# Kernel tuning notes

Measured on AMD Instinct MI355X. Metric: run time of the kernel, lower is better.

The kernel has to match this reference:

```python
import jax, jax.numpy as jnp
import numpy as np

DM = 768            # d_model
DI = 1536           # d_inner = expand * d_model
P = 64              # headdim
H = DI // P         # 24 heads
N = 64              # d_state (Mamba2Simple default)
K = 4               # d_conv
CONVD = DI + 2 * N  # 1664
D_IN_PROJ = 2 * DI + 2 * N + H  # 3224
BATCH = 2
NVAL = 1024
L = NVAL
EPS = 1e-5

# static tail_order / swap_order index (transpose the rows x cols token grid, reversed)
_rows = int(NVAL ** 0.5)
_t = np.arange(NVAL).reshape(_rows, -1).T
_t = NVAL - 1 - _t
TAIL = _t.reshape(-1)
SEQ = jnp.asarray(np.concatenate([np.arange(L - NVAL), TAIL + (L - NVAL)]))


def _make_params(key, prefix):
    ks = jax.random.split(key, 6)
    dt = jnp.exp(jax.random.uniform(ks[2], (H,), minval=np.log(1e-3), maxval=np.log(1e-1)))
    return {
        prefix + 'ln_w': jnp.ones(DM, jnp.float32),
        prefix + 'ln_b': jnp.zeros(DM, jnp.float32),
        prefix + 'in_w': jax.random.normal(ks[0], (D_IN_PROJ, DM), jnp.float32) * 0.02,
        prefix + 'conv_w': jax.random.normal(ks[1], (CONVD, K), jnp.float32) * 0.1,
        prefix + 'conv_b': jnp.zeros(CONVD, jnp.float32),
        prefix + 'dt_bias': jnp.log(jnp.expm1(dt)),  # inverse softplus of dt in [1e-3, 1e-1]
        prefix + 'A_log': jnp.log(jax.random.uniform(ks[3], (H,), minval=1.0, maxval=16.0)),
        prefix + 'D': jnp.ones(H, jnp.float32),
        prefix + 'norm_w': jnp.ones(DI, jnp.float32),
        prefix + 'out_w': jax.random.normal(ks[4], (DM, DI), jnp.float32) * 0.02,
    }


def setup_inputs() -> dict:
    key = jax.random.key(0)
    k1, k2, k3 = jax.random.split(key, 3)
    inp = {'x': jax.random.normal(k1, (BATCH, L, DM), dtype=jnp.float32)}
    inp.update(_make_params(k2, 'f_'))
    inp.update(_make_params(k3, 'b_'))
    return inp


def _layernorm(x, w, b):
    m = jnp.mean(x, -1, keepdims=True)
    v = jnp.mean((x - m) ** 2, -1, keepdims=True)
    return (x - m) * jax.lax.rsqrt(v + EPS) * w + b


def _mamba2(x, in_w, conv_w, conv_b, dt_bias, A_log, Dp, norm_w, out_w):
    Bsz, Lseq, _ = x.shape
    zxbcdt = x @ in_w.T                                   # [B,L,3224]
    z, xBC, dt = jnp.split(zxbcdt, [DI, DI + CONVD], axis=-1)
    dt = jax.nn.softplus(dt + dt_bias)                    # [B,L,H]
    # causal depthwise conv1d over channels
    xc = jnp.transpose(xBC, (0, 2, 1))                    # [B,C,L]
    xc = jax.lax.conv_general_dilated(xc, conv_w[:, None, :], (1,), [(K - 1, 0)],
                                      feature_group_count=CONVD)
    xBC = jax.nn.silu(jnp.transpose(xc, (0, 2, 1)) + conv_b)
    xs, Bm, Cm = jnp.split(xBC, [DI, DI + N], axis=-1)
    xs = xs.reshape(Bsz, Lseq, H, P)
    A = -jnp.exp(A_log)                                   # [H], negative

    def step(S, inp):
        dt_t, x_t, B_t, C_t = inp                         # [B,H],[B,H,P],[B,N],[B,N]
        dA = jnp.exp(dt_t * A)                            # [B,H]
        S = S * dA[..., None, None] + dt_t[..., None, None] * B_t[:, None, :, None] * x_t[:, :, None, :]
        y = jnp.einsum('bn,bhnp->bhp', C_t, S)
        return S, y

    S0 = jnp.zeros((Bsz, H, N, P), x.dtype)
    ins = (jnp.moveaxis(dt, 1, 0), jnp.moveaxis(xs, 1, 0),
           jnp.moveaxis(Bm, 1, 0), jnp.moveaxis(Cm, 1, 0))
    _, ys = jax.lax.scan(step, S0, ins)
    y = jnp.moveaxis(ys, 0, 1) + Dp[None, None, :, None] * xs  # D skip, [B,L,H,P]
    y = y.reshape(Bsz, Lseq, DI)
    # RMSNormGated: gate then rmsnorm
    y = y * jax.nn.silu(z)
    y = y * jax.lax.rsqrt(jnp.mean(y * y, -1, keepdims=True) + EPS) * norm_w
    return y @ out_w.T


def _wrap(x, ln_w, ln_b, *mp):
    return x + _mamba2(_layernorm(x, ln_w, ln_b), *mp)


def reference(x,
              f_ln_w, f_ln_b, f_in_w, f_conv_w, f_conv_b, f_dt_bias, f_A_log, f_D, f_norm_w, f_out_w,
              b_ln_w, b_ln_b, b_in_w, b_conv_w, b_conv_b, b_dt_bias, b_A_log, b_D, b_norm_w, b_out_w):
    left_right = _wrap(x, f_ln_w, f_ln_b, f_in_w, f_conv_w, f_conv_b, f_dt_bias, f_A_log, f_D, f_norm_w, f_out_w)
    xs = x[:, SEQ]
    down_up = _wrap(xs, b_ln_w, b_ln_b, b_in_w, b_conv_w, b_conv_b, b_dt_bias, b_A_log, b_D, b_norm_w, b_out_w)
    down_up = down_up[:, SEQ]
    return left_right + down_up
```

## Files before the change

kernel.cpp:

```cpp
#include <hip/hip_runtime.h>
#include <cstdint>

#define DM    768
#define DI    1536
#define PP    64
#define HH    24
#define NN    64
#define CONVD 1664
#define DINP  3224
#define NP1   3328
#define LL    1024
#define ROWS  2048
#define EPSF  1e-5f
#define NCHUNK 16
#define CLEN   64

typedef unsigned short ushortT;
typedef __attribute__((ext_vector_type(8))) __bf16 bf16x8;
typedef __attribute__((ext_vector_type(8))) unsigned short ushort8;
typedef __attribute__((ext_vector_type(4))) float f32x4;

__device__ __forceinline__ int seqmap(int t) { return 1023 - 32 * (t & 31) - (t >> 5); }

__device__ __forceinline__ ushortT f2bf(float f) {
  union { float f; unsigned u; } v; v.f = f;
  unsigned r = v.u + 0x7FFF + ((v.u >> 16) & 1);
  return (ushortT)(r >> 16);
}
__device__ __forceinline__ float bf2f(ushortT b) {
  union { unsigned u; float f; } v; v.u = ((unsigned)b) << 16;
  return v.f;
}

__device__ __forceinline__ void gload_lds16(const void* g, void* l) {
  __builtin_amdgcn_global_load_lds((const __attribute__((address_space(1))) void*)g,
                                   (__attribute__((address_space(3))) void*)l, 16, 0, 0);
}

#define SWZ(r, c) ((r) * 64 + ((c) ^ (((r) & 7) << 3)))
#define SWZ64(r, c) ((r) * 64 + ((c) ^ (((r) & 7) << 3)))

__global__ __launch_bounds__(256) void cvt_all_kernel(
    const float* __restrict__ fw1, const float* __restrict__ bw1,
    const float* __restrict__ fw2, const float* __restrict__ bw2,
    ushortT* __restrict__ WP1, ushortT* __restrict__ W2) {
  const long NW1 = (long)NP1 * DM, SW1 = (long)DINP * DM, NW2 = (long)DM * DI;
  const long tot8 = (2 * NW1 + 2 * NW2) >> 3;
  for (long i8 = (long)blockIdx.x * 256 + threadIdx.x; i8 < tot8; i8 += (long)gridDim.x * 256) {
    long i = i8 << 3;
    const float* src = nullptr;
    ushortT* dst;
    if (i < NW1) {
      if (i < SW1) src = fw1 + i;
      dst = WP1 + i;
    } else if (i < 2 * NW1) {
      long j = i - NW1;
      if (j < SW1) src = bw1 + j;
      dst = WP1 + i;
    } else if (i < 2 * NW1 + NW2) {
      long j = i - 2 * NW1;
      src = fw2 + j;
      dst = W2 + j;
    } else {
      long j = i - 2 * NW1 - NW2;
      src = bw2 + j;
      dst = W2 + NW2 + j;
    }
    ushort8 o = {};
    if (src) {
      float4 a = *(const float4*)src;
      float4 b2 = *(const float4*)(src + 4);
      o[0] = f2bf(a.x);  o[1] = f2bf(a.y);  o[2] = f2bf(a.z);  o[3] = f2bf(a.w);
      o[4] = f2bf(b2.x); o[5] = f2bf(b2.y); o[6] = f2bf(b2.z); o[7] = f2bf(b2.w);
    }
    *(ushort8*)dst = o;
  }
}

__global__ __launch_bounds__(256) void ln_kernel(const float* __restrict__ x,
    const float* __restrict__ wf, const float* __restrict__ bf_,
    const float* __restrict__ wb, const float* __restrict__ bb,
    ushortT* __restrict__ xln) {
  __shared__ float lds[4];
  int bid = blockIdx.x;
  int dir = bid >> 11, row = bid & 2047;
  int b = row >> 10, t = row & 1023;
  int st = dir ? seqmap(t) : t;
  const float* xr = x + (size_t)(b * 1024 + st) * DM;
  const float* w = dir ? wb : wf;
  const float* bia = dir ? bb : bf_;
  int tid = threadIdx.x;
  float v0 = xr[tid], v1 = xr[tid + 256], v2 = xr[tid + 512];
  float s = v0 + v1 + v2;
  #pragma unroll
  for (int o = 32; o; o >>= 1) s += __shfl_xor(s, o, 64);
  if ((tid & 63) == 0) lds[tid >> 6] = s;
  __syncthreads();
  float mean = (lds[0] + lds[1] + lds[2] + lds[3]) * (1.f / 768.f);
  __syncthreads();
  float d0 = v0 - mean, d1 = v1 - mean, d2 = v2 - mean;
  float q = d0 * d0 + d1 * d1 + d2 * d2;
  #pragma unroll
  for (int o = 32; o; o >>= 1) q += __shfl_xor(q, o, 64);
  if ((tid & 63) == 0) lds[tid >> 6] = q;
  __syncthreads();
  float var = (lds[0] + lds[1] + lds[2] + lds[3]) * (1.f / 768.f);
  float rs = rsqrtf(var + EPSF);
  ushortT* orow = xln + (size_t)bid * DM;
  orow[tid]       = f2bf(d0 * rs * w[tid]       + bia[tid]);
  orow[tid + 256] = f2bf(d1 * rs * w[tid + 256] + bia[tid + 256]);
  orow[tid + 512] = f2bf(d2 * rs * w[tid + 512] + bia[tid + 512]);
}

template<int MODE>
__global__ __launch_bounds__(256) void gemm_bf16(
    const ushortT* __restrict__ Aall, const ushortT* __restrict__ Ball,
    float* __restrict__ Cfall, ushortT* __restrict__ Cball,
    int K, int lda, int ldb, int ldc, long sA, long sB, long sCf, long sCb) {
  __shared__ ushortT sA2[2][128 * 64];
  __shared__ ushortT sB2[2][128 * 64];
  int gx = gridDim.x, gy = gridDim.y;
  int nwg = gx * gy * gridDim.z;
  int lid = blockIdx.x + gx * (blockIdx.y + gy * blockIdx.z);
  int cpx = nwg >> 3;
  int swz = (lid & 7) * cpx + (lid >> 3);
  int bx = swz % gx;
  int rest = swz / gx;
  int by = rest % gy, bz = rest / gy;
  const ushortT* A = Aall + (size_t)bz * sA;
  const ushortT* B = Ball + (size_t)bz * sB;
  int tid = threadIdx.x, lane = tid & 63, w = tid >> 6;
  int wm = w >> 1, wn = w & 1;
  int m0 = by * 128, n0 = bx * 128;
  int rA8 = lane >> 3;
  int cSw = ((lane & 7) << 3) ^ (((lane >> 3) & 7) << 3);
  f32x4 acc[4][4] = {};
  const int NT = K >> 6;
  int fr = lane & 15, kq = lane >> 4;

  auto STAGE = [&](int bf, int kt) {
    int kc = kt * 64 + cSw;
    #pragma unroll
    for (int c2 = 0; c2 < 4; ++c2) {
      int q = w * 4 + c2;
      gload_lds16(A + (size_t)(m0 + q * 8 + rA8) * lda + kc, &sA2[bf][q * 512]);
    }
    #pragma unroll
    for (int c2 = 0; c2 < 4; ++c2) {
      int q = w * 4 + c2;
      gload_lds16(B + (size_t)(n0 + q * 8 + rA8) * ldb + kc, &sB2[bf][q * 512]);
    }
  };

  STAGE(0, 0);
  int cur = 0;
  for (int kt = 0; kt < NT; ++kt) {
    if (kt + 1 < NT) {
      STAGE(cur ^ 1, kt + 1);
      asm volatile("s_waitcnt vmcnt(8)" ::: "memory");
    } else {
      asm volatile("s_waitcnt vmcnt(0)" ::: "memory");
    }
    __builtin_amdgcn_s_barrier();
    __builtin_amdgcn_sched_barrier(0);
    #pragma unroll
    for (int ks = 0; ks < 2; ++ks) {
      int kb = ks * 32 + kq * 8;
      bf16x8 af[4], bfr[4];
      #pragma unroll
      for (int i = 0; i < 4; ++i)
        af[i] = *(const bf16x8*)&sA2[cur][SWZ64(wm * 64 + i * 16 + fr, kb)];
      #pragma unroll
      for (int j = 0; j < 4; ++j)
        bfr[j] = *(const bf16x8*)&sB2[cur][SWZ64(wn * 64 + j * 16 + fr, kb)];
      #pragma unroll
      for (int i = 0; i < 4; ++i)
        #pragma unroll
        for (int j = 0; j < 4; ++j)
          acc[i][j] = __builtin_amdgcn_mfma_f32_16x16x32_bf16(af[i], bfr[j], acc[i][j], 0, 0, 0);
    }
    asm volatile("s_waitcnt lgkmcnt(0)" ::: "memory");
    __builtin_amdgcn_sched_barrier(0);
    __builtin_amdgcn_s_barrier();
    cur ^= 1;
  }
  int cr = (lane >> 4) * 4, cc = lane & 15;
  if (MODE == 1 && n0 >= 3200) {
    float* Cf = Cfall + (size_t)bz * sCf;
    #pragma unroll
    for (int i = 0; i < 4; ++i)
      #pragma unroll
      for (int j = 0; j < 4; ++j) {
        float* Cp = Cf + (size_t)(m0 + wm * 64 + i * 16 + cr) * 128 + (wn * 64 + j * 16 + cc);
        #pragma unroll
        for (int r = 0; r < 4; ++r) Cp[(size_t)r * 128] = acc[i][j][r];
      }
  } else {
    ushortT* Cb = Cball + (size_t)bz * sCb;
    #pragma unroll
    for (int i = 0; i < 4; ++i)
      #pragma unroll
      for (int j = 0; j < 4; ++j) {
        ushortT* Cp = Cb + (size_t)(m0 + wm * 64 + i * 16 + cr) * ldc + (n0 + wn * 64 + j * 16 + cc);
        #pragma unroll
        for (int r = 0; r < 4; ++r) Cp[(size_t)r * ldc] = f2bf(acc[i][j][r]);
      }
  }
}

__global__ __launch_bounds__(256) void conv_dt_kernel(const ushortT* __restrict__ zxb,
    const float* __restrict__ dtt,
    const float* __restrict__ cwf, const float* __restrict__ cbf,
    const float* __restrict__ cwb, const float* __restrict__ cbb,
    const float* __restrict__ dtbf, const float* __restrict__ alogf,
    const float* __restrict__ dtbb, const float* __restrict__ alogb,
    ushortT* __restrict__ xcb, float* __restrict__ dts, float* __restrict__ lda_) {
  int bid = blockIdx.x;
  int dir = bid >> 11, row = bid & 2047;
  int t = row & 1023;
  const float* cw   = dir ? cwb : cwf;
  const float* cb   = dir ? cbb : cbf;
  const float* dtb  = dir ? dtbb : dtbf;
  const float* alog = dir ? alogb : alogf;
  const ushortT* zrow = zxb + (size_t)bid * NP1;
  int tid = threadIdx.x;
  if (tid < HH) {
    float raw = dtt[(size_t)bid * 128 + tid] + dtb[tid];
    float dtv = raw > 20.f ? raw : log1pf(expf(raw));
    dts[(size_t)bid * HH + tid] = dtv;
    lda_[(size_t)bid * HH + tid] = -expf(alog[tid]) * dtv;
  }
  ushortT* xrow = xcb + (size_t)bid * CONVD;
  for (int c = tid; c < CONVD; c += 256) {
    float acc = cb[c];
    #pragma unroll
    for (int k = 0; k < 4; ++k) {
      int tt = t - 3 + k;
      if (tt >= 0) acc += bf2f(zrow[(long)(k - 3) * NP1 + 1536 + c]) * cw[c * 4 + k];
    }
    xrow[c] = f2bf(acc / (1.f + expf(-acc)));
  }
}

__global__ __launch_bounds__(256) void ssd_chunk_kernel(const ushortT* __restrict__ xcb,
    const float* __restrict__ dts, const float* __restrict__ lda_,
    ushortT* __restrict__ yb, ushortT* __restrict__ slocb, float* __restrict__ cwg,
    ushortT* __restrict__ cbg) {
  __shared__ ushortT sCb[4096];
  __shared__ ushortT sBb[4096];
  __shared__ ushortT sBT[4096];
  __shared__ ushortT sXT[4096];
  __shared__ ushortT sMb[4096];
  __shared__ float clog[64];
  __shared__ float dt64[64];
  __shared__ float wv64[64];
  int gh = blockIdx.x;
  int c  = blockIdx.y;
  int dir = gh / 48;
  int rem = gh % 48;
  int b = rem / 24, h = rem % 24;
  int tid = threadIdx.x, lane = tid & 63;
  int w = tid >> 6;
  size_t rowbase = ((size_t)dir * 2 + b) * 1024;
  size_t trow = rowbase + (size_t)c * CLEN;

  #pragma unroll
  for (int it2 = 0; it2 < 2; ++it2) {
    int idx2 = it2 * 256 + tid;
    int r = idx2 >> 3, c8 = (idx2 & 7) << 3;
    const ushortT* xrow = xcb + (trow + r) * CONVD;
    *(ushort8*)&sCb[SWZ(r, c8)] = *(const ushort8*)&xrow[1600 + c8];
    *(ushort8*)&sBb[SWZ(r, c8)] = *(const ushort8*)&xrow[1536 + c8];
  }
  #pragma unroll
  for (int it = 0; it < 16; ++it) {
    int idx = it * 256 + tid;
    int r = idx >> 6, cc = idx & 63;
    sXT[SWZ(cc, r)] = xcb[(trow + r) * CONVD + h * 64 + cc];
  }
  if (tid < 64) {
    float ld = lda_[(trow + tid) * HH + h];
    float dtv = dts[(trow + tid) * HH + h];
    float v = ld;
    #pragma unroll
    for (int o = 1; o < 64; o <<= 1) {
      float u = __shfl_up(v, o, 64);
      if (tid >= o) v += u;
    }
    float tot = __shfl(v, 63, 64);
    clog[tid] = v;
    dt64[tid] = dtv;
    wv64[tid] = dtv * __expf(tot - v);
    cwg[(trow + tid) * HH + h] = __expf(v);
  }
  __syncthreads();

  if (h == 0) {
    ushortT* dst = cbg + ((size_t)((dir * 2 + b) * NCHUNK + c)) * 4096;
    for (int idx = tid; idx < 4096; idx += 256) dst[idx] = sCb[idx];
  }

  int fr = lane & 15, kq = lane >> 4;

  #pragma unroll
  for (int it = 0; it < 16; ++it) {
    int idx = it * 256 + tid;
    int s = idx >> 6, n = idx & 63;
    float bv = bf2f(sBb[SWZ(s, n)]) * wv64[s];
    sBT[SWZ(n, s)] = f2bf(bv);
  }
  f32x4 accG[4] = {};
  #pragma unroll
  for (int kt = 0; kt < 2; ++kt) {
    int kk = kt * 32 + kq * 8;
    bf16x8 af = *(const bf16x8*)&sCb[SWZ(w * 16 + fr, kk)];
    #pragma unroll
    for (int j = 0; j < 4; ++j) {
      bf16x8 bf_ = *(const bf16x8*)&sBb[SWZ(j * 16 + fr, kk)];
      accG[j] = __builtin_amdgcn_mfma_f32_16x16x32_bf16(af, bf_, accG[j], 0, 0, 0);
    }
  }
  #pragma unroll
  for (int j = 0; j < 4; ++j) {
    int s = j * 16 + fr;
    float cls = clog[s], dtv = dt64[s];
    #pragma unroll
    for (int r = 0; r < 4; ++r) {
      int t = w * 16 + kq * 4 + r;
      float dec = (s <= t) ? __expf(clog[t] - cls) * dtv : 0.f;
      sMb[SWZ(t, s)] = f2bf(accG[j][r] * dec);
    }
  }
  __syncthreads();

  f32x4 accY[4] = {}, accS[4] = {};
  #pragma unroll
  for (int kt = 0; kt < 2; ++kt) {
    int kk = kt * 32 + kq * 8;
    bf16x8 aM = *(const bf16x8*)&sMb[SWZ(w * 16 + fr, kk)];
    bf16x8 aB = *(const bf16x8*)&sBT[SWZ(w * 16 + fr, kk)];
    #pragma unroll
    for (int j = 0; j < 4; ++j) {
      bf16x8 bx = *(const bf16x8*)&sXT[SWZ(j * 16 + fr, kk)];
      accY[j] = __builtin_amdgcn_mfma_f32_16x16x32_bf16(aM, bx, accY[j], 0, 0, 0);
      accS[j] = __builtin_amdgcn_mfma_f32_16x16x32_bf16(aB, bx, accS[j], 0, 0, 0);
    }
  }
  ushortT* spb = slocb + ((size_t)gh * NCHUNK + c) * 4096;
  #pragma unroll
  for (int j = 0; j < 4; ++j) {
    #pragma unroll
    for (int r = 0; r < 4; ++r) {
      int t = w * 16 + kq * 4 + r;
      int p = j * 16 + fr;
      yb[(trow + t) * DI + h * 64 + p] = f2bf(accY[j][r]);
      spb[t * 64 + p] = f2bf(accS[j][r]);
    }
  }
}

__global__ __launch_bounds__(256) void chunk_prefix_kernel(
    const ushortT* __restrict__ slocb, const float* __restrict__ cwg,
    ushortT* __restrict__ sinitb) {
  __shared__ float ldsT[64 * 65];
  int gh = blockIdx.x;
  int dir = gh / 48;
  int rem = gh % 48;
  int b = rem / 24, h = rem % 24;
  int tid = threadIdx.x;
  size_t rowbase = ((size_t)dir * 2 + b) * 1024;
  float R[16];
  #pragma unroll
  for (int j = 0; j < 16; ++j) R[j] = 0.f;
  for (int c = 1; c < NCHUNK; ++c) {
    float W = cwg[(rowbase + (size_t)c * CLEN - 1) * HH + h];
    const ushortT* slot = slocb + ((size_t)gh * NCHUNK + (c - 1)) * 4096;
    #pragma unroll
    for (int j = 0; j < 16; ++j) {
      int idx = j * 256 + tid, n = idx >> 6, p = idx & 63;
      R[j] = __builtin_fmaf(R[j], W, bf2f(slot[idx]));
      ldsT[n * 65 + p] = R[j];
    }
    __syncthreads();
    ushortT* outp = sinitb + ((size_t)gh * (NCHUNK - 1) + (c - 1)) * 4096;
    #pragma unroll
    for (int j = 0; j < 16; ++j) {
      int idx = j * 256 + tid, p = idx >> 6, n = idx & 63;
      outp[SWZ(p, n)] = f2bf(ldsT[n * 65 + p]);
    }
    __syncthreads();
  }
}

__global__ __launch_bounds__(256) void fixup_kernel(
    const ushortT* __restrict__ cbg, const ushortT* __restrict__ sinitb,
    const float* __restrict__ cwg, ushortT* __restrict__ yib) {
  __shared__ ushortT sCb[4096];
  __shared__ ushortT sST[4096];
  int gh = blockIdx.x;
  int c = blockIdx.y + 1;
  int dir = gh / 48;
  int rem = gh % 48;
  int b = rem / 24, h = rem % 24;
  int tid = threadIdx.x, lane = tid & 63, w = tid >> 6;
  size_t rowbase = ((size_t)dir * 2 + b) * 1024;
  size_t trow = rowbase + (size_t)c * CLEN;
  const ushortT* cbSrc = cbg + ((size_t)((dir * 2 + b) * NCHUNK + c)) * 4096;
  const ushortT* stSrc = sinitb + ((size_t)gh * (NCHUNK - 1) + (c - 1)) * 4096;
  #pragma unroll
  for (int ph = 0; ph < 2; ++ph) {
    int base = ph * 2048 + w * 512;
    gload_lds16(cbSrc + base + lane * 8, &sCb[base]);
    gload_lds16(stSrc + base + lane * 8, &sST[base]);
  }
  __syncthreads();
  int fr = lane & 15, kq = lane >> 4;
  f32x4 accY[4] = {};
  #pragma unroll
  for (int kt = 0; kt < 2; ++kt) {
    int kk = kt * 32 + kq * 8;
    bf16x8 aC = *(const bf16x8*)&sCb[SWZ(w * 16 + fr, kk)];
    #pragma unroll
    for (int j = 0; j < 4; ++j) {
      bf16x8 bS = *(const bf16x8*)&sST[SWZ(j * 16 + fr, kk)];
      accY[j] = __builtin_amdgcn_mfma_f32_16x16x32_bf16(aC, bS, accY[j], 0, 0, 0);
    }
  }
  float cwv[4];
  #pragma unroll
  for (int r = 0; r < 4; ++r)
    cwv[r] = cwg[(trow + w * 16 + kq * 4 + r) * HH + h];
  #pragma unroll
  for (int j = 0; j < 4; ++j)
    #pragma unroll
    for (int r = 0; r < 4; ++r) {
      int t = w * 16 + kq * 4 + r, p = j * 16 + fr;
      yib[(trow + t) * DI + h * 64 + p] = f2bf(accY[j][r] * cwv[r]);
    }
}

__global__ __launch_bounds__(256) void gate_norm_kernel(
    const ushortT* __restrict__ yb, const ushortT* __restrict__ yib,
    const ushortT* __restrict__ zxb, const ushortT* __restrict__ xcb,
    const float* __restrict__ Df, const float* __restrict__ Db,
    const float* __restrict__ nwf, const float* __restrict__ nwb,
    ushortT* __restrict__ yn) {
  __shared__ float lds[4];
  int bid = blockIdx.x;
  int dir = bid >> 11;
  int t = bid & 1023;
  const float* Dp = dir ? Db : Df;
  const float* nw = dir ? nwb : nwf;
  int tid = threadIdx.x;
  bool act = tid < 192;
  int c0 = tid * 8;
  float v[8];
  float ss = 0.f;
  if (act) {
    ushort8 yv8 = *(const ushort8*)&yb[(size_t)bid * DI + c0];
    ushort8 zv8 = *(const ushort8*)&zxb[(size_t)bid * NP1 + c0];
    ushort8 xv8 = *(const ushort8*)&xcb[(size_t)bid * CONVD + c0];
    ushort8 yi8 = {};
    bool hasI = (t >= CLEN);
    if (hasI) yi8 = *(const ushort8*)&yib[(size_t)bid * DI + c0];
    float Dv = Dp[c0 >> 6];
    #pragma unroll
    for (int e = 0; e < 8; ++e) {
      float yv = bf2f(yv8[e]) + (hasI ? bf2f(yi8[e]) : 0.f) + Dv * bf2f(xv8[e]);
      float zv = bf2f(zv8[e]);
      yv *= zv / (1.f + expf(-zv));
      v[e] = yv;
      ss += yv * yv;
    }
  }
  #pragma unroll
  for (int o = 32; o; o >>= 1) ss += __shfl_xor(ss, o, 64);
  if ((tid & 63) == 0) lds[tid >> 6] = ss;
  __syncthreads();
  float ms = (lds[0] + lds[1] + lds[2] + lds[3]) * (1.f / 1536.f);
  float sc = rsqrtf(ms + EPSF);
  if (act) {
    ushort8 o8;
    #pragma unroll
    for (int e = 0; e < 8; ++e) o8[e] = f2bf(v[e] * sc * nw[c0 + e]);
    *(ushort8*)&yn[(size_t)bid * DI + c0] = o8;
  }
}

__global__ __launch_bounds__(128) void combine_kernel(const float* __restrict__ x,
    const ushortT* __restrict__ mf, const ushortT* __restrict__ mb,
    float* __restrict__ out) {
  int bid = blockIdx.x;
  int b = bid >> 10, t = bid & 1023;
  int st = seqmap(t);
  int tid = threadIdx.x;
  if (tid >= 96) return;
  int c0 = tid * 8;
  ushort8 fv = *(const ushort8*)&mf[(size_t)bid * DM + c0];
  ushort8 bv = *(const ushort8*)&mb[(size_t)(b * 1024 + st) * DM + c0];
  const float4 x0 = *(const float4*)&x[(size_t)bid * DM + c0];
  const float4 x1 = *(const float4*)&x[(size_t)bid * DM + c0 + 4];
  float4 o0, o1;
  o0.x = 2.f * x0.x + bf2f(fv[0]) + bf2f(bv[0]);
  o0.y = 2.f * x0.y + bf2f(fv[1]) + bf2f(bv[1]);
  o0.z = 2.f * x0.z + bf2f(fv[2]) + bf2f(bv[2]);
  o0.w = 2.f * x0.w + bf2f(fv[3]) + bf2f(bv[3]);
  o1.x = 2.f * x1.x + bf2f(fv[4]) + bf2f(bv[4]);
  o1.y = 2.f * x1.y + bf2f(fv[5]) + bf2f(bv[5]);
  o1.z = 2.f * x1.z + bf2f(fv[6]) + bf2f(bv[6]);
  o1.w = 2.f * x1.w + bf2f(fv[7]) + bf2f(bv[7]);
  *(float4*)&out[(size_t)bid * DM + c0] = o0;
  *(float4*)&out[(size_t)bid * DM + c0 + 4] = o1;
}

extern "C" void kernel_launch(void* const* d_in, const int* in_sizes, int n_in,
                              void* d_out, int out_size, void* d_ws, size_t ws_size,
                              hipStream_t stream) {
  const float* x       = (const float*)d_in[0];
  const float* f_ln_w  = (const float*)d_in[1];
  const float* f_ln_b  = (const float*)d_in[2];
  const float* f_in_w  = (const float*)d_in[3];
  const float* f_cw    = (const float*)d_in[4];
  const float* f_cb    = (const float*)d_in[5];
  const float* f_dtb   = (const float*)d_in[6];
  const float* f_alog  = (const float*)d_in[7];
  const float* f_D     = (const float*)d_in[8];
  const float* f_nw    = (const float*)d_in[9];
  const float* f_ow    = (const float*)d_in[10];
  const float* b_ln_w  = (const float*)d_in[11];
  const float* b_ln_b  = (const float*)d_in[12];
  const float* b_in_w  = (const float*)d_in[13];
  const float* b_cw    = (const float*)d_in[14];
  const float* b_cb    = (const float*)d_in[15];
  const float* b_dtb   = (const float*)d_in[16];
  const float* b_alog  = (const float*)d_in[17];
  const float* b_D     = (const float*)d_in[18];
  const float* b_nw    = (const float*)d_in[19];
  const float* b_ow    = (const float*)d_in[20];

  char* ws = (char*)d_ws;
  size_t off = 0;
  auto carve = [&](size_t bytes) -> char* {
    off = (off + 255) & ~(size_t)255;
    char* p = ws + off;
    off += bytes;
    return p;
  };
  ushortT* XLN   = (ushortT*)carve((size_t)2 * ROWS * DM * 2);
  ushortT* WP1   = (ushortT*)carve((size_t)2 * NP1 * DM * 2);
  ushortT* W2    = (ushortT*)carve((size_t)2 * DM * DI * 2);
  ushortT* ZXB   = (ushortT*)carve((size_t)2 * ROWS * NP1 * 2);
  float*   DTT   = (float*)carve((size_t)2 * ROWS * 128 * 4);
  ushortT* XCB   = (ushortT*)carve((size_t)2 * ROWS * CONVD * 2);
  float*   DTS   = (float*)carve((size_t)2 * ROWS * HH * 4);
  float*   LDA   = (float*)carve((size_t)2 * ROWS * HH * 4);
  ushortT* YB    = (ushortT*)carve((size_t)2 * ROWS * DI * 2);
  ushortT* YIB   = (ushortT*)carve((size_t)2 * ROWS * DI * 2);
  ushortT* YN    = (ushortT*)carve((size_t)2 * ROWS * DI * 2);
  ushortT* MOUTB = (ushortT*)carve((size_t)2 * ROWS * DM * 2);
  ushortT* SLOCB = (ushortT*)carve((size_t)96 * NCHUNK * 4096 * 2);
  ushortT* SINIB = (ushortT*)carve((size_t)96 * (NCHUNK - 1) * 4096 * 2);
  ushortT* CBG   = (ushortT*)carve((size_t)4 * NCHUNK * 4096 * 2);
  float*   CWG   = (float*)carve((size_t)2 * ROWS * HH * 4);

  cvt_all_kernel<<<2048, 256, 0, stream>>>(f_in_w, b_in_w, f_ow, b_ow, WP1, W2);

  ln_kernel<<<4096, 256, 0, stream>>>(x, f_ln_w, f_ln_b, b_ln_w, b_ln_b, XLN);

  gemm_bf16<1><<<dim3(NP1 / 128, ROWS / 128, 2), 256, 0, stream>>>(
      XLN, WP1, DTT, ZXB, DM, DM, DM, NP1,
      (long)ROWS * DM, (long)NP1 * DM, (long)ROWS * 128, (long)ROWS * NP1);

  conv_dt_kernel<<<4096, 256, 0, stream>>>(ZXB, DTT, f_cw, f_cb, b_cw, b_cb,
                                           f_dtb, f_alog, b_dtb, b_alog,
                                           XCB, DTS, LDA);

  ssd_chunk_kernel<<<dim3(96, NCHUNK), 256, 0, stream>>>(XCB, DTS, LDA, YB, SLOCB, CWG, CBG);
  chunk_prefix_kernel<<<96, 256, 0, stream>>>(SLOCB, CWG, SINIB);
  fixup_kernel<<<dim3(96, NCHUNK - 1), 256, 0, stream>>>(CBG, SINIB, CWG, YIB);

  gate_norm_kernel<<<4096, 256, 0, stream>>>(YB, YIB, ZXB, XCB, f_D, b_D, f_nw, b_nw, YN);

  gemm_bf16<0><<<dim3(DM / 128, ROWS / 128, 2), 256, 0, stream>>>(
      YN, W2, nullptr, MOUTB, DI, DI, DI, DM,
      (long)ROWS * DI, (long)DM * DI, 0, (long)ROWS * DM);

  combine_kernel<<<2048, 128, 0, stream>>>(x, MOUTB, MOUTB + (size_t)ROWS * DM, (float*)d_out);
}
```

Before: 164.6 us.

## Triple-buffer GEMM, tile conv via LDS, vectorize SSD transposes, trim gate_norm block

The bf16 GEMM goes from double to triple buffering of its LDS tiles, so loads are issued two k-steps ahead with matching vmcnt waits. The conv/dt kernel is restructured from one block per row into blocks that each stage a 67-row by 208-channel stripe in LDS and compute the causal conv with 8-wide vector loads and stores. In the SSD chunk kernel the X and B transposes now write four elements per LDS store instead of scalar stores. gate_norm launches 192 threads so no threads sit idle. The GEMM now uses 96KB of LDS, which may lower occupancy.

```diff
diff --git a/kernel.cpp b/kernel.cpp
--- a/kernel.cpp
+++ b/kernel.cpp
@@ -14,10 +14,12 @@
 #define EPSF  1e-5f
 #define NCHUNK 16
 #define CLEN   64
+#define CSTRIPE 208
 
 typedef unsigned short ushortT;
 typedef __attribute__((ext_vector_type(8))) __bf16 bf16x8;
 typedef __attribute__((ext_vector_type(8))) unsigned short ushort8;
+typedef __attribute__((ext_vector_type(4))) unsigned short ushort4v;
 typedef __attribute__((ext_vector_type(4))) float f32x4;
 
 __device__ __forceinline__ int seqmap(int t) { return 1023 - 32 * (t & 31) - (t >> 5); }
@@ -117,8 +119,8 @@
     const ushortT* __restrict__ Aall, const ushortT* __restrict__ Ball,
     float* __restrict__ Cfall, ushortT* __restrict__ Cball,
     int K, int lda, int ldb, int ldc, long sA, long sB, long sCf, long sCb) {
-  __shared__ ushortT sA2[2][128 * 64];
-  __shared__ ushortT sB2[2][128 * 64];
+  __shared__ ushortT sA3[3][128 * 64];
+  __shared__ ushortT sB3[3][128 * 64];
   int gx = gridDim.x, gy = gridDim.y;
   int nwg = gx * gy * gridDim.z;
   int lid = blockIdx.x + gx * (blockIdx.y + gy * blockIdx.z);
@@ -143,36 +145,39 @@
     #pragma unroll
     for (int c2 = 0; c2 < 4; ++c2) {
       int q = w * 4 + c2;
-      gload_lds16(A + (size_t)(m0 + q * 8 + rA8) * lda + kc, &sA2[bf][q * 512]);
+      gload_lds16(A + (size_t)(m0 + q * 8 + rA8) * lda + kc, &sA3[bf][q * 512]);
     }
     #pragma unroll
     for (int c2 = 0; c2 < 4; ++c2) {
       int q = w * 4 + c2;
-      gload_lds16(B + (size_t)(n0 + q * 8 + rA8) * ldb + kc, &sB2[bf][q * 512]);
+      gload_lds16(B + (size_t)(n0 + q * 8 + rA8) * ldb + kc, &sB3[bf][q * 512]);
     }
   };
 
   STAGE(0, 0);
-  int cur = 0;
+  if (NT > 1) STAGE(1, 1);
   for (int kt = 0; kt < NT; ++kt) {
-    if (kt + 1 < NT) {
-      STAGE(cur ^ 1, kt + 1);
+    if (kt + 2 < NT) {
+      STAGE((kt + 2) % 3, kt + 2);
+      asm volatile("s_waitcnt vmcnt(16)" ::: "memory");
+    } else if (kt + 2 == NT) {
       asm volatile("s_waitcnt vmcnt(8)" ::: "memory");
     } else {
       asm volatile("s_waitcnt vmcnt(0)" ::: "memory");
     }
     __builtin_amdgcn_s_barrier();
     __builtin_amdgcn_sched_barrier(0);
+    int cur = kt % 3;
     #pragma unroll
     for (int ks = 0; ks < 2; ++ks) {
       int kb = ks * 32 + kq * 8;
       bf16x8 af[4], bfr[4];
       #pragma unroll
       for (int i = 0; i < 4; ++i)
-        af[i] = *(const bf16x8*)&sA2[cur][SWZ64(wm * 64 + i * 16 + fr, kb)];
+        af[i] = *(const bf16x8*)&sA3[cur][SWZ64(wm * 64 + i * 16 + fr, kb)];
       #pragma unroll
       for (int j = 0; j < 4; ++j)
-        bfr[j] = *(const bf16x8*)&sB2[cur][SWZ64(wn * 64 + j * 16 + fr, kb)];
+        bfr[j] = *(const bf16x8*)&sB3[cur][SWZ64(wn * 64 + j * 16 + fr, kb)];
       #pragma unroll
       for (int i = 0; i < 4; ++i)
         #pragma unroll
@@ -182,7 +187,6 @@
     asm volatile("s_waitcnt lgkmcnt(0)" ::: "memory");
     __builtin_amdgcn_sched_barrier(0);
     __builtin_amdgcn_s_barrier();
-    cur ^= 1;
   }
   int cr = (lane >> 4) * 4, cc = lane & 15;
   if (MODE == 1 && n0 >= 3200) {
@@ -215,30 +219,52 @@
     const float* __restrict__ dtbf, const float* __restrict__ alogf,
     const float* __restrict__ dtbb, const float* __restrict__ alogb,
     ushortT* __restrict__ xcb, float* __restrict__ dts, float* __restrict__ lda_) {
-  int bid = blockIdx.x;
-  int dir = bid >> 11, row = bid & 2047;
-  int t = row & 1023;
-  const float* cw   = dir ? cwb : cwf;
-  const float* cb   = dir ? cbb : cbf;
-  const float* dtb  = dir ? dtbb : dtbf;
-  const float* alog = dir ? alogb : alogf;
-  const ushortT* zrow = zxb + (size_t)bid * NP1;
+  __shared__ ushortT sZ[67][CSTRIPE];
+  int stripe = blockIdx.x, chunk = blockIdx.y, dirb = blockIdx.z;
+  int dir = dirb >> 1;
+  int t0 = chunk * 64;
+  size_t rowb = (size_t)dirb * 1024;
+  const float* cw = dir ? cwb : cwf;
+  const float* cb = dir ? cbb : cbf;
   int tid = threadIdx.x;
-  if (tid < HH) {
-    float raw = dtt[(size_t)bid * 128 + tid] + dtb[tid];
-    float dtv = raw > 20.f ? raw : log1pf(expf(raw));
-    dts[(size_t)bid * HH + tid] = dtv;
-    lda_[(size_t)bid * HH + tid] = -expf(alog[tid]) * dtv;
-  }
-  ushortT* xrow = xcb + (size_t)bid * CONVD;
-  for (int c = tid; c < CONVD; c += 256) {
-    float acc = cb[c];
-    #pragma unroll
-    for (int k = 0; k < 4; ++k) {
-      int tt = t - 3 + k;
-      if (tt >= 0) acc += bf2f(zrow[(long)(k - 3) * NP1 + 1536 + c]) * cw[c * 4 + k];
-    }
-    xrow[c] = f2bf(acc / (1.f + expf(-acc)));
+  int cbase = stripe * CSTRIPE;
+  for (int idx = tid; idx < 67 * 26; idx += 256) {
+    int r = idx / 26, u = idx % 26;
+    int t = t0 - 3 + r;
+    ushort8 v = {};
+    if (t >= 0)
+      v = *(const ushort8*)&zxb[(rowb + t) * NP1 + 1536 + cbase + u * 8];
+    *(ushort8*)&sZ[r][u * 8] = v;
+  }
+  if (stripe == 0) {
+    const float* dtb  = dir ? dtbb : dtbf;
+    const float* alog = dir ? alogb : alogf;
+    for (int i = tid; i < 64 * HH; i += 256) {
+      int tt = i / HH, h = i % HH;
+      size_t row = rowb + t0 + tt;
+      float raw = dtt[row * 128 + h] + dtb[h];
+      float dtv = raw > 20.f ? raw : log1pf(expf(raw));
+      dts[row * HH + h] = dtv;
+      lda_[row * HH + h] = -expf(alog[h]) * dtv;
+    }
+  }
+  __syncthreads();
+  for (int idx = tid; idx < 64 * 26; idx += 256) {
+    int r = idx / 26, u = idx % 26;
+    int c0 = cbase + u * 8;
+    ushort8 x0 = *(const ushort8*)&sZ[r][u * 8];
+    ushort8 x1 = *(const ushort8*)&sZ[r + 1][u * 8];
+    ushort8 x2 = *(const ushort8*)&sZ[r + 2][u * 8];
+    ushort8 x3 = *(const ushort8*)&sZ[r + 3][u * 8];
+    ushort8 o;
+    #pragma unroll
+    for (int e = 0; e < 8; ++e) {
+      int c = c0 + e;
+      float acc = cb[c] + bf2f(x0[e]) * cw[c * 4 + 0] + bf2f(x1[e]) * cw[c * 4 + 1]
+                + bf2f(x2[e]) * cw[c * 4 + 2] + bf2f(x3[e]) * cw[c * 4 + 3];
+      o[e] = f2bf(acc / (1.f + expf(-acc)));
+    }
+    *(ushort8*)&xcb[(rowb + t0 + r) * CONVD + c0] = o;
   }
 }
 
@@ -272,11 +298,19 @@
     *(ushort8*)&sCb[SWZ(r, c8)] = *(const ushort8*)&xrow[1600 + c8];
     *(ushort8*)&sBb[SWZ(r, c8)] = *(const ushort8*)&xrow[1536 + c8];
   }
-  #pragma unroll
-  for (int it = 0; it < 16; ++it) {
-    int idx = it * 256 + tid;
-    int r = idx >> 6, cc = idx & 63;
-    sXT[SWZ(cc, r)] = xcb[(trow + r) * CONVD + h * 64 + cc];
+  {
+    int p = lane;
+    #pragma unroll
+    for (int q = 0; q < 4; ++q) {
+      int t4 = w * 16 + q * 4;
+      ushortT a0 = xcb[(trow + t4 + 0) * CONVD + h * 64 + p];
+      ushortT a1 = xcb[(trow + t4 + 1) * CONVD + h * 64 + p];
+      ushortT a2 = xcb[(trow + t4 + 2) * CONVD + h * 64 + p];
+      ushortT a3 = xcb[(trow + t4 + 3) * CONVD + h * 64 + p];
+      int cT = t4 ^ ((p & 7) << 3);
+      ushort4v v4 = {a0, a1, a2, a3};
+      *(ushort4v*)&sXT[p * 64 + cT] = v4;
+    }
   }
   if (tid < 64) {
     float ld = lda_[(trow + tid) * HH + h];
@@ -302,12 +336,19 @@
 
   int fr = lane & 15, kq = lane >> 4;
 
-  #pragma unroll
-  for (int it = 0; it < 16; ++it) {
-    int idx = it * 256 + tid;
-    int s = idx >> 6, n = idx & 63;
-    float bv = bf2f(sBb[SWZ(s, n)]) * wv64[s];
-    sBT[SWZ(n, s)] = f2bf(bv);
+  {
+    int n = lane;
+    #pragma unroll
+    for (int q = 0; q < 4; ++q) {
+      int s4 = w * 16 + q * 4;
+      float b0 = bf2f(sBb[SWZ(s4 + 0, n)]) * wv64[s4 + 0];
+      float b1 = bf2f(sBb[SWZ(s4 + 1, n)]) * wv64[s4 + 1];
+      float b2 = bf2f(sBb[SWZ(s4 + 2, n)]) * wv64[s4 + 2];
+      float b3 = bf2f(sBb[SWZ(s4 + 3, n)]) * wv64[s4 + 3];
+      int cT = s4 ^ ((n & 7) << 3);
+      ushort4v v4 = {f2bf(b0), f2bf(b1), f2bf(b2), f2bf(b3)};
+      *(ushort4v*)&sBT[n * 64 + cT] = v4;
+    }
   }
   f32x4 accG[4] = {};
   #pragma unroll
@@ -439,24 +480,23 @@
     }
 }
 
-__global__ __launch_bounds__(256) void gate_norm_kernel(
+__global__ __launch_bounds__(192) void gate_norm_kernel(
     const ushortT* __restrict__ yb, const ushortT* __restrict__ yib,
     const ushortT* __restrict__ zxb, const ushortT* __restrict__ xcb,
     const float* __restrict__ Df, const float* __restrict__ Db,
     const float* __restrict__ nwf, const float* __restrict__ nwb,
     ushortT* __restrict__ yn) {
-  __shared__ float lds[4];
+  __shared__ float lds[3];
   int bid = blockIdx.x;
   int dir = bid >> 11;
   int t = bid & 1023;
   const float* Dp = dir ? Db : Df;
   const float* nw = dir ? nwb : nwf;
   int tid = threadIdx.x;
-  bool act = tid < 192;
   int c0 = tid * 8;
   float v[8];
   float ss = 0.f;
-  if (act) {
+  {
     ushort8 yv8 = *(const ushort8*)&yb[(size_t)bid * DI + c0];
     ushort8 zv8 = *(const ushort8*)&zxb[(size_t)bid * NP1 + c0];
     ushort8 xv8 = *(const ushort8*)&xcb[(size_t)bid * CONVD + c0];
@@ -477,9 +517,9 @@
   for (int o = 32; o; o >>= 1) ss += __shfl_xor(ss, o, 64);
   if ((tid & 63) == 0) lds[tid >> 6] = ss;
   __syncthreads();
-  float ms = (lds[0] + lds[1] + lds[2] + lds[3]) * (1.f / 1536.f);
+  float ms = (lds[0] + lds[1] + lds[2]) * (1.f / 1536.f);
   float sc = rsqrtf(ms + EPSF);
-  if (act) {
+  {
     ushort8 o8;
     #pragma unroll
     for (int e = 0; e < 8; ++e) o8[e] = f2bf(v[e] * sc * nw[c0 + e]);
@@ -571,15 +611,15 @@
       XLN, WP1, DTT, ZXB, DM, DM, DM, NP1,
       (long)ROWS * DM, (long)NP1 * DM, (long)ROWS * 128, (long)ROWS * NP1);
 
-  conv_dt_kernel<<<4096, 256, 0, stream>>>(ZXB, DTT, f_cw, f_cb, b_cw, b_cb,
-                                           f_dtb, f_alog, b_dtb, b_alog,
-                                           XCB, DTS, LDA);
+  conv_dt_kernel<<<dim3(8, 16, 4), 256, 0, stream>>>(ZXB, DTT, f_cw, f_cb, b_cw, b_cb,
+                                                     f_dtb, f_alog, b_dtb, b_alog,
+                                                     XCB, DTS, LDA);
 
   ssd_chunk_kernel<<<dim3(96, NCHUNK), 256, 0, stream>>>(XCB, DTS, LDA, YB, SLOCB, CWG, CBG);
   chunk_prefix_kernel<<<96, 256, 0, stream>>>(SLOCB, CWG, SINIB);
   fixup_kernel<<<dim3(96, NCHUNK - 1), 256, 0, stream>>>(CBG, SINIB, CWG, YIB);
 
-  gate_norm_kernel<<<4096, 256, 0, stream>>>(YB, YIB, ZXB, XCB, f_D, b_D, f_nw, b_nw, YN);
+  gate_norm_kernel<<<4096, 192, 0, stream>>>(YB, YIB, ZXB, XCB, f_D, b_D, f_nw, b_nw, YN);
 
   gemm_bf16<0><<<dim3(DM / 128, ROWS / 128, 2), 256, 0, stream>>>(
       YN, W2, nullptr, MOUTB, DI, DI, DI, DM,
```

New measurement: 187.2 us. 13.7% more time.
